# Performance work log

Measured on AMD Instinct MI355X. Metric: run time of the kernel, lower is better.

## Reference

```python
import jax, jax.numpy as jnp
import numpy as np

# param tuples: (vdecay, vth, grad_win(=threshold_adaptation), grad_amp, rate_scale)
HID = (0.5, 0.3, 0.3, 1.0, 1.0)
OUT = (0.5, 0.3, 0.3, 1.0, 1.0)

B, I, H, O, T = 128, 1024, 4096, 512, 100


def setup_inputs() -> dict:
    key = jax.random.key(0)
    k1, k2, k3 = jax.random.split(key, 3)
    return {
        "spike_data": jax.random.uniform(k1, (B, I, T), dtype=jnp.float32),
        "hid_spike0": jnp.zeros((B, H), jnp.float32),
        "hid_volt0": jnp.zeros((B, H), jnp.float32),
        "out_spike0": jnp.zeros((B, O), jnp.float32),
        "out_volt0": jnp.zeros((B, O), jnp.float32),
        "w_hid": jax.random.normal(k2, (H, I), dtype=jnp.float32) * 0.02,
        "w_out": jax.random.normal(k3, (O, H), dtype=jnp.float32) * 0.02,
        "batch_size": B,
        "spike_ts": T,
    }


def _spike(volt, p):
    vdecay, vth, grad_win, grad_amp, rate_scale = p
    scaled = rate_scale * volt
    dyn_vth = vth * jnp.tanh(grad_win * jnp.max(scaled))
    return (scaled > dyn_vth).astype(volt.dtype)


def reference(spike_data, hid_spike0, hid_volt0, out_spike0, out_volt0,
              w_hid, w_out, batch_size, spike_ts):
    x = jnp.transpose(spike_data.reshape(batch_size, I, spike_ts), (2, 0, 1))  # [T,B,I]

    def step(carry, xt):
        hs, hv, osp, ov = carry
        hv_new = hv * HID[0] * (1.0 - hs) + xt @ w_hid.T          # [B,H]
        hs_new = _spike(hv_new, HID)
        ov_new = ov * OUT[0] * (1.0 - osp) + hs_new @ w_out.T     # [B,O]
        os_new = _spike(ov_new, OUT)
        return (hs_new, hv_new, os_new, ov_new), os_new

    _, outs = jax.lax.scan(step, (hid_spike0, hid_volt0, out_spike0, out_volt0), x)
    return jnp.sum(outs, axis=0)  # [B,O]
```

## Files before the change

### kernel.cpp

```cpp
#include <hip/hip_runtime.h>
#include <math.h>
#include <stdint.h>

#define T_STEPS 100
#define B_DIM 128
#define I_DIM 1024
#define H_DIM 4096
#define O_DIM 512
#define T_CHUNK 20
#define HS_RING 21
#define HS_SLOT ((size_t)8*128*512)
#define OV_LAG 21
#define RING_S 40
#define TAIL_START 80
#define LEADER 255

typedef _Float16 f16x8 __attribute__((ext_vector_type(8)));
typedef _Float16 f16x4 __attribute__((ext_vector_type(4)));
typedef float    f32x4 __attribute__((ext_vector_type(4)));

#define AS1 __attribute__((address_space(1)))
#define AS3 __attribute__((address_space(3)))

#define ALOAD(p)    __hip_atomic_load((p), __ATOMIC_RELAXED, __HIP_MEMORY_SCOPE_AGENT)
#define ASTORE(p,v) __hip_atomic_store((p), (v), __ATOMIC_RELAXED, __HIP_MEMORY_SCOPE_AGENT)

__device__ __forceinline__ void gload_lds16(const _Float16* g, _Float16* l){
  __builtin_amdgcn_global_load_lds(
      (const AS1 unsigned*)(uintptr_t)g,
      (AS3 unsigned*)(unsigned)(uintptr_t)l, 16, 0, 0);
}

__device__ __forceinline__ unsigned fmap(float f){
  unsigned u = __float_as_uint(f);
  return (u & 0x80000000u) ? ~u : (u | 0x80000000u);
}
__device__ __forceinline__ float funmap(unsigned m){
  unsigned u = (m & 0x80000000u) ? (m & 0x7FFFFFFFu) : ~m;
  return __uint_as_float(u);
}
__device__ __forceinline__ float vth_of(unsigned m){
  return 0.3f * tanhf(0.3f * funmap(m));
}

__device__ __forceinline__ unsigned poll2max(const unsigned* base, int idx){
  const unsigned long long* p = (const unsigned long long*)base + idx;
  unsigned long long v = ALOAD(p);
  while (((unsigned)v) == 0u || ((unsigned)(v >> 32)) == 0u){
    __builtin_amdgcn_s_sleep(1);
    v = ALOAD(p);
  }
  unsigned lo = (unsigned)v, hi = (unsigned)(v >> 32);
  return lo > hi ? lo : hi;
}
__device__ __forceinline__ unsigned wred_umax(unsigned v){
  #pragma unroll
  for (int o = 32; o > 0; o >>= 1){
    unsigned t = (unsigned)__shfl_down((int)v, o);
    if (t > v) v = t;
  }
  return v;
}

__global__ __launch_bounds__(256) void init_kernel(float* hv, float* ovs,
                                                   uint32_t* cnt32,
                                                   unsigned* hmaxA, unsigned* omaxA,
                                                   unsigned* hflag, unsigned* oflag,
                                                   unsigned* otflag)
{
  int i = blockIdx.x * 256 + threadIdx.x;
  if (i < B_DIM*H_DIM) hv[i] = 0.f;
  if (i < B_DIM*O_DIM) ovs[i] = 0.f;
  if (i < B_DIM*O_DIM/4) cnt32[i] = 0u;
  if (i < 100*256) hflag[i] = 0u;
  if (i < 101*32)  oflag[i] = 0u;
  if (i < 20*128)  otflag[i] = 0u;
  if (i < 128){
    unsigned v = (i==0) ? 0x80000000u : 0u;
    hmaxA[i] = v; omaxA[i] = v;
  }
}

__global__ __launch_bounds__(256) void prep_x(const float* __restrict__ sp,
                                              _Float16* __restrict__ Ahi,
                                              _Float16* __restrict__ Alo, int t0)
{
  __shared__ float tile[32][16][10];
  const int b16 = blockIdx.x, kc = blockIdx.y, tz = blockIdx.z;
  for (int e = threadIdx.x; e < 5120; e += 256){
    int tt = e % 10, row = e / 10;
    int bb = row >> 5, ii = row & 31;
    tile[ii][bb][tt] =
      sp[((size_t)(b16*16+bb)*I_DIM + kc*32 + ii)*T_STEPS + t0 + tz*10 + tt];
  }
  __syncthreads();
  for (int u = threadIdx.x; u < 640; u += 256){
    int tl = u >> 6, l = u & 63, kg = l >> 4, r = l & 15;
    f16x8 hi, lo;
    #pragma unroll
    for (int e=0;e<8;e++){
      float x = tile[kg*8+e][r][tl] * 2048.f;
      _Float16 h = (_Float16)x;
      hi[e] = h;
      lo[e] = (_Float16)(x - (float)h);
    }
    int t_local = tz*10 + tl;
    size_t off = ((size_t)(t_local*8 + b16)*32 + kc)*512 + kg*128 + r*8;
    *(f16x8*)(Ahi + off) = hi;
    *(f16x8*)(Alo + off) = lo;
  }
}

__global__ __launch_bounds__(256) void prep_weights(
    const float* __restrict__ Wh, const float* __restrict__ Wo,
    _Float16* __restrict__ WHhi, _Float16* __restrict__ WHlo,
    _Float16* __restrict__ WOhi, _Float16* __restrict__ WOlo)
{
  const int blk = blockIdx.x;
  if (blk < 256){
    const int n16 = blk;
    for (int u = threadIdx.x; u < 2048; u += 256){
      int kc = u >> 6, l = u & 63, kg = l >> 4, r = l & 15;
      const float* src = Wh + (size_t)(n16*16 + r)*I_DIM + kc*32 + kg*8;
      f16x8 hi, lo;
      #pragma unroll
      for (int e=0;e<8;e++){
        float x = src[e] * 256.f;
        _Float16 h = (_Float16)x;
        hi[e] = h; lo[e] = (_Float16)(x - (float)h);
      }
      size_t off = ((size_t)n16*32 + kc)*512 + kg*128 + r*8;
      *(f16x8*)(WHhi + off) = hi;
      *(f16x8*)(WHlo + off) = lo;
    }
  } else {
    const int n16 = blk - 256;
    for (int u = threadIdx.x; u < 8192; u += 256){
      int kc = u >> 6, l = u & 63, kg = l >> 4, r = l & 15;
      const float* src = Wo + (size_t)(n16*16 + r)*H_DIM + kc*32 + kg*8;
      f16x8 hi, lo;
      #pragma unroll
      for (int e=0;e<8;e++){
        float x = src[e] * 256.f;
        _Float16 h = (_Float16)x;
        hi[e] = h; lo[e] = (_Float16)(x - (float)h);
      }
      size_t off = ((size_t)(n16*128 + kc))*512 + kg*128 + r*8;
      *(f16x8*)(WOhi + off) = hi;
      *(f16x8*)(WOlo + off) = lo;
    }
  }
}

__global__ __launch_bounds__(256, 2) void gemm1_mfma(
    const _Float16* __restrict__ Ahi, const _Float16* __restrict__ Alo,
    const _Float16* __restrict__ Bhi, const _Float16* __restrict__ Blo,
    float* __restrict__ G)
{
  __shared__ __align__(16) _Float16 lds[2][4][8][512];
  const int tid = threadIdx.x, wave = tid>>6, lane = tid&63;
  const int bn = blockIdx.x, bm = blockIdx.y;
  const int wm = wave>>1, wn = wave&1;

  const _Float16* srcbase = (wave==0)?Ahi:(wave==1)?Alo:(wave==2)?Bhi:Blo;
  const int r16b = ((wave<2) ? bm : bn)*8;
  const _Float16* gsrc = srcbase + (size_t)r16b*32*512 + lane*8;

  f32x4 acc[16];
  #pragma unroll
  for (int i=0;i<16;i++) acc[i] = (f32x4){0.f,0.f,0.f,0.f};

  #pragma unroll
  for (int q=0;q<8;q++)
    gload_lds16(gsrc + (size_t)q*32*512, &lds[0][wave][q][0]);

  for (int kc=0;kc<32;kc++){
    __syncthreads();
    if (kc < 31){
      #pragma unroll
      for (int q=0;q<8;q++)
        gload_lds16(gsrc + ((size_t)q*32 + kc+1)*512, &lds[(kc+1)&1][wave][q][0]);
    }
    const int cb = kc&1;
    f16x8 fAh[4], fAl[4], fBh[4], fBl[4];
    #pragma unroll
    for (int i=0;i<4;i++){
      fAh[i] = *(const f16x8*)&lds[cb][0][wm*4+i][lane*8];
      fAl[i] = *(const f16x8*)&lds[cb][1][wm*4+i][lane*8];
      fBh[i] = *(const f16x8*)&lds[cb][2][wn*4+i][lane*8];
      fBl[i] = *(const f16x8*)&lds[cb][3][wn*4+i][lane*8];
    }
    #pragma unroll
    for (int i=0;i<4;i++)
      #pragma unroll
      for (int j=0;j<4;j++)
        acc[i*4+j] = __builtin_amdgcn_mfma_f32_16x16x32_f16(fAh[i], fBh[j], acc[i*4+j], 0,0,0);
    #pragma unroll
    for (int i=0;i<4;i++)
      #pragma unroll
      for (int j=0;j<4;j++)
        acc[i*4+j] = __builtin_amdgcn_mfma_f32_16x16x32_f16(fAh[i], fBl[j], acc[i*4+j], 0,0,0);
    #pragma unroll
    for (int i=0;i<4;i++)
      #pragma unroll
      for (int j=0;j<4;j++)
        acc[i*4+j] = __builtin_amdgcn_mfma_f32_16x16x32_f16(fAl[i], fBh[j], acc[i*4+j], 0,0,0);
  }
  const int colw = lane&15, quad = lane>>4;
  const float sc = 1.f/(2048.f*256.f);
  float* eds = (float*)lds + wave*2048;
  __syncthreads();
  #pragma unroll
  for (int ih=0; ih<2; ih++){
    #pragma unroll
    for (int il=0; il<2; il++){
      int i = ih*2+il;
      #pragma unroll
      for (int j=0;j<4;j++)
        #pragma unroll
        for (int r=0;r<4;r++)
          eds[(il*16 + quad*4 + r)*64 + j*16 + colw] = acc[i*4+j][r]*sc;
    }
    #pragma unroll
    for (int rr8=0; rr8<8; rr8++){
      int row = rr8*4 + quad;
      float4 v = *(float4*)&eds[row*64 + colw*4];
      int m = bm*128 + wm*64 + ih*32 + row;
      int n = bn*128 + wn*64 + colw*4;
      *(float4*)&G[(size_t)m*H_DIM + n] = v;
    }
  }
}

__global__ __launch_bounds__(256) void hv_step(
    const float* __restrict__ Gs, float* __restrict__ hv,
    _Float16* __restrict__ hs_slot,
    const unsigned* __restrict__ hmax_t, unsigned* __restrict__ hmax_n, int t,
    const float* __restrict__ OGp, float* __restrict__ ovs,
    uchar4* __restrict__ cnt8, unsigned* __restrict__ omaxA, int ovt)
{
  __shared__ float red[4];
  const int tid = threadIdx.x, lane = tid&63, wv = tid>>6;

  if (blockIdx.x < 512){
    if (t > T_STEPS) return;
    const int gid = blockIdx.x*256 + tid;
    const int b = gid >> 10, h0 = (gid & 1023) << 2;
    const float vth = vth_of(*hmax_t);
    float4 h = *(const float4*)(hv + (size_t)gid*4);

    if (t > 0){
      const int kc = h0>>5, kg=(h0>>3)&3, e=h0&7, r=b&15, m16l=b>>4;
      f16x4 s;
      s[0]=(h.x>vth)?(_Float16)1:(_Float16)0; s[1]=(h.y>vth)?(_Float16)1:(_Float16)0;
      s[2]=(h.z>vth)?(_Float16)1:(_Float16)0; s[3]=(h.w>vth)?(_Float16)1:(_Float16)0;
      *(f16x4*)(hs_slot + ((size_t)m16l*128 + kc)*512 + kg*128 + r*8 + e) = s;
    }
    if (t < T_STEPS){
      float4 g = *(const float4*)(Gs + (size_t)gid*4);
      float4 o;
      o.x = (h.x>vth ? 0.f : 0.5f*h.x) + g.x;
      o.y = (h.y>vth ? 0.f : 0.5f*h.y) + g.y;
      o.z = (h.z>vth ? 0.f : 0.5f*h.z) + g.z;
      o.w = (h.w>vth ? 0.f : 0.5f*h.w) + g.w;
      *(float4*)(hv + (size_t)gid*4) = o;
      float lmax = fmaxf(fmaxf(o.x,o.y),fmaxf(o.z,o.w));
      #pragma unroll
      for (int off=32; off>0; off>>=1) lmax = fmaxf(lmax, __shfl_down(lmax, off));
      if (lane==0) red[wv] = lmax;
      __syncthreads();
      if (tid==0){
        float m = fmaxf(fmaxf(red[0],red[1]),fmaxf(red[2],red[3]));
        atomicMax(hmax_n, fmap(m));
      }
    }
  } else {
    if (ovt < 0 || ovt >= TAIL_START) return;
    const int f = (int)(blockIdx.x - 512)*256 + tid;
    const float vthp = vth_of(omaxA[ovt]);
    const int slot = ovt % RING_S;
    float lmax = -3.0e38f;
    #pragma unroll
    for (int q=0;q<4;q++){
      int o4 = f + q*4096;
      float4 v = *(const float4*)(ovs + (size_t)o4*4);
      uchar4 c = cnt8[o4];
      bool s0 = v.x > vthp, s1 = v.y > vthp, s2 = v.z > vthp, s3 = v.w > vthp;
      c.x += s0; c.y += s1; c.z += s2; c.w += s3;
      v.x = s0 ? 0.f : 0.5f*v.x;
      v.y = s1 ? 0.f : 0.5f*v.y;
      v.z = s2 ? 0.f : 0.5f*v.z;
      v.w = s3 ? 0.f : 0.5f*v.w;
      float4 g0 = *(const float4*)(OGp + ((size_t)slot*4+0)*(B_DIM*O_DIM) + (size_t)o4*4);
      float4 g1 = *(const float4*)(OGp + ((size_t)slot*4+1)*(B_DIM*O_DIM) + (size_t)o4*4);
      float4 g2 = *(const float4*)(OGp + ((size_t)slot*4+2)*(B_DIM*O_DIM) + (size_t)o4*4);
      float4 g3 = *(const float4*)(OGp + ((size_t)slot*4+3)*(B_DIM*O_DIM) + (size_t)o4*4);
      v.x += (g0.x+g1.x)+(g2.x+g3.x);
      v.y += (g0.y+g1.y)+(g2.y+g3.y);
      v.z += (g0.z+g1.z)+(g2.z+g3.z);
      v.w += (g0.w+g1.w)+(g2.w+g3.w);
      lmax = fmaxf(lmax, fmaxf(fmaxf(v.x,v.y),fmaxf(v.z,v.w)));
      *(float4*)(ovs + (size_t)o4*4) = v;
      cnt8[o4] = c;
    }
    #pragma unroll
    for (int off=32; off>0; off>>=1) lmax = fmaxf(lmax, __shfl_down(lmax, off));
    if (lane==0) red[wv] = lmax;
    __syncthreads();
    if (tid==0){
      float m = fmaxf(fmaxf(red[0],red[1]),fmaxf(red[2],red[3]));
      atomicMax(&omaxA[ovt+1], fmap(m));
    }
  }
}

__global__ __launch_bounds__(512) void hv_chunk(
    const float* __restrict__ Gs,
    float* __restrict__ hv,
    _Float16* __restrict__ HS,
    unsigned* __restrict__ hmaxA,
    const float* __restrict__ OGp, float* __restrict__ ovs,
    uchar4* __restrict__ cnt8, unsigned* __restrict__ omaxA,
    unsigned* __restrict__ hflag, unsigned* __restrict__ oflag,
    int t0, int nsteps)
{
  __shared__ float red[8], redo[8];
  __shared__ unsigned sredH[2];
  __shared__ unsigned sredO;
  const int tid = threadIdx.x, lane = tid&63, wv = tid>>6;
  const int blk = blockIdx.x;
  const int gid = blk*512 + tid;
  const int b = gid >> 10, h0 = (gid & 1023) << 2;
  const int kc = h0>>5, kg=(h0>>3)&3, e=h0&7, r=b&15, m16l=b>>4;
  const bool ovblk = blk < 32;
  const int ovt0 = t0 - OV_LAG;
  const bool rid = ovblk && (ovt0 >= 0);

  float4 h = *(const float4*)(hv + (size_t)gid*4);
  float4 vo = make_float4(0.f,0.f,0.f,0.f);
  unsigned cw = 0;
  if (ovblk){
    vo = *(const float4*)(ovs + (size_t)gid*4);
    uchar4 c0 = cnt8[gid];
    cw = (unsigned)c0.x | ((unsigned)c0.y<<8) | ((unsigned)c0.z<<16) | ((unsigned)c0.w<<24);
  }
  float4 g = *(const float4*)(Gs + (size_t)gid*4);
  unsigned hm_cur = hmaxA[t0];
  unsigned om_cur = rid ? omaxA[ovt0] : 0;

  float4 og0,og1,og2,og3;
  og0=og1=og2=og3=make_float4(0.f,0.f,0.f,0.f);
  if (rid){
    const int sl = ovt0 % RING_S;
    const float* base = OGp + (size_t)gid*4;
    og0 = *(const float4*)(base + (size_t)(sl*4+0)*(B_DIM*O_DIM));
    og1 = *(const float4*)(base + (size_t)(sl*4+1)*(B_DIM*O_DIM));
    og2 = *(const float4*)(base + (size_t)(sl*4+2)*(B_DIM*O_DIM));
    og3 = *(const float4*)(base + (size_t)(sl*4+3)*(B_DIM*O_DIM));
  }

  for (int j = 0; j < nsteps; j++){
    const int t = t0 + j;
    const int ovt = t - OV_LAG;
    const bool last = (j == nsteps-1);

    float4 gn = make_float4(0.f,0.f,0.f,0.f);
    if (!last && (t+1) < T_STEPS)
      gn = *(const float4*)(Gs + (size_t)(j+1)*(B_DIM*H_DIM) + (size_t)gid*4);
    float4 on0,on1,on2,on3;
    on0=on1=on2=on3=make_float4(0.f,0.f,0.f,0.f);
    if (rid && !last){
      const int sln = (ovt+1) % RING_S;
      const float* base = OGp + (size_t)gid*4;
      on0 = *(const float4*)(base + (size_t)(sln*4+0)*(B_DIM*O_DIM));
      on1 = *(const float4*)(base + (size_t)(sln*4+1)*(B_DIM*O_DIM));
      on2 = *(const float4*)(base + (size_t)(sln*4+2)*(B_DIM*O_DIM));
      on3 = *(const float4*)(base + (size_t)(sln*4+3)*(B_DIM*O_DIM));
    }

    const float vth = vth_of(hm_cur);
    {
      f16x4 s;
      s[0]=(h.x>vth)?(_Float16)1:(_Float16)0; s[1]=(h.y>vth)?(_Float16)1:(_Float16)0;
      s[2]=(h.z>vth)?(_Float16)1:(_Float16)0; s[3]=(h.w>vth)?(_Float16)1:(_Float16)0;
      _Float16* slotp = HS + (size_t)((t-1)%HS_RING)*HS_SLOT;
      *(f16x4*)(slotp + ((size_t)m16l*128 + kc)*512 + kg*128 + r*8 + e) = s;
    }
    float lmax = -3.0e38f;
    if (t < T_STEPS){
      h.x = (h.x>vth ? 0.f : 0.5f*h.x) + g.x;
      h.y = (h.y>vth ? 0.f : 0.5f*h.y) + g.y;
      h.z = (h.z>vth ? 0.f : 0.5f*h.z) + g.z;
      h.w = (h.w>vth ? 0.f : 0.5f*h.w) + g.w;
      lmax = fmaxf(fmaxf(h.x,h.y),fmaxf(h.z,h.w));
    }

    float omax_l = -3.0e38f;
    if (rid){
      const float vthp = vth_of(om_cur);
      bool s0 = vo.x > vthp, s1 = vo.y > vthp, s2 = vo.z > vthp, s3 = vo.w > vthp;
      cw += (s0?1u:0u) | (s1?(1u<<8):0u) | (s2?(1u<<16):0u) | (s3?(1u<<24):0u);
      vo.x = s0 ? 0.f : 0.5f*vo.x;
      vo.y = s1 ? 0.f : 0.5f*vo.y;
      vo.z = s2 ? 0.f : 0.5f*vo.z;
      vo.w = s3 ? 0.f : 0.5f*vo.w;
      vo.x += (og0.x+og1.x)+(og2.x+og3.x);
      vo.y += (og0.y+og1.y)+(og2.y+og3.y);
      vo.z += (og0.z+og1.z)+(og2.z+og3.z);
      vo.w += (og0.w+og1.w)+(og2.w+og3.w);
      omax_l = fmaxf(fmaxf(vo.x,vo.y),fmaxf(vo.z,vo.w));
    }

    #pragma unroll
    for (int off2=32; off2>0; off2>>=1) lmax = fmaxf(lmax, __shfl_down(lmax, off2));
    if (lane==0) red[wv] = lmax;
    if (rid){
      #pragma unroll
      for (int off2=32; off2>0; off2>>=1) omax_l = fmaxf(omax_l, __shfl_down(omax_l, off2));
      if (lane==0) redo[wv] = omax_l;
    }
    __syncthreads();

    if (tid == 0 && t < T_STEPS){
      float m = red[0];
      #pragma unroll
      for (int w2=1; w2<8; w2++) m = fmaxf(m, red[w2]);
      ASTORE(&hflag[(size_t)t*256 + blk], fmap(m));
    }
    if (tid == 0 && rid){
      float mo = redo[0];
      #pragma unroll
      for (int w2=1; w2<8; w2++) mo = fmaxf(mo, redo[w2]);
      ASTORE(&oflag[(size_t)ovt*32 + blk], fmap(mo));
    }

    if (!last){
      if (tid < 128){
        unsigned mx = poll2max(hflag + (size_t)t*256, tid);
        mx = wred_umax(mx);
        if (lane == 0) sredH[wv] = mx;
      }
      if (rid && tid >= 128 && tid < 192){
        unsigned mx = 0;
        if (tid < 144) mx = poll2max(oflag + (size_t)ovt*32, tid - 128);
        mx = wred_umax(mx);
        if (lane == 0) sredO = mx;
      }
      __syncthreads();
      { unsigned m0 = sredH[0], m1 = sredH[1];
        hm_cur = m0 > m1 ? m0 : m1; }
      if (rid) om_cur = sredO;
      if (blk == LEADER && tid == 0) ASTORE(&hmaxA[t+1], hm_cur);
      if (blk == 0 && rid && tid == 0) ASTORE(&omaxA[ovt+1], om_cur);
      g = gn;
      og0=on0; og1=on1; og2=on2; og3=on3;
    } else {
      if (blk == LEADER && t < T_STEPS){
        if (tid < 128){
          unsigned mx = poll2max(hflag + (size_t)t*256, tid);
          mx = wred_umax(mx);
          if (lane == 0) sredH[wv] = mx;
        }
        __syncthreads();
        if (tid == 0){
          unsigned m0 = sredH[0], m1 = sredH[1];
          ASTORE(&hmaxA[t+1], m0 > m1 ? m0 : m1);
        }
      }
      if (blk == 0 && rid){
        if (tid < 64){
          unsigned mx = 0;
          if (tid < 16) mx = poll2max(oflag + (size_t)ovt*32, tid);
          mx = wred_umax(mx);
          if (tid == 0) ASTORE(&omaxA[ovt+1], mx);
        }
      }
    }
  }

  *(float4*)(hv + (size_t)gid*4) = h;
  if (ovblk){
    *(float4*)(ovs + (size_t)gid*4) = vo;
    cnt8[gid] = make_uchar4((unsigned char)(cw & 0xffu),
                            (unsigned char)((cw>>8) & 0xffu),
                            (unsigned char)((cw>>16) & 0xffu),
                            (unsigned char)((cw>>24) & 0xffu));
  }
}

__global__ __launch_bounds__(256, 2) void gemm2_mfma(
    const _Float16* __restrict__ HS,
    const _Float16* __restrict__ WoHi, const _Float16* __restrict__ WoLo,
    float* __restrict__ OGp, int c)
{
  __shared__ __align__(16) _Float16 lds2[2][24][512];
  const int tid = threadIdx.x, wave = tid>>6, lane = tid&63;
  const int bn = blockIdx.x, bm = blockIdx.y, kh = blockIdx.z;
  const int s = c*T_CHUNK + bm, ring = s % HS_RING;
  const int wm = wave>>1, wn = wave&1;
  const int kc0 = kh*32;

  const _Float16* baseA = HS   + (size_t)ring*8*128*512 + lane*8;
  const _Float16* baseH = WoHi + (size_t)bn*8*128*512 + lane*8;
  const _Float16* baseL = WoLo + (size_t)bn*8*128*512 + lane*8;

  f32x4 acc[16];
  #pragma unroll
  for (int i=0;i<16;i++) acc[i] = (f32x4){0.f,0.f,0.f,0.f};

  #pragma unroll
  for (int i=0;i<6;i++){
    int f = wave*6 + i;
    const _Float16* g = (f<8)  ? baseA + ((size_t)f*128      + kc0)*512
                     : (f<16) ? baseH + ((size_t)(f-8)*128  + kc0)*512
                              : baseL + ((size_t)(f-16)*128 + kc0)*512;
    gload_lds16(g, &lds2[0][f][0]);
  }

  for (int k=0;k<32;k++){
    __syncthreads();
    if (k < 31){
      #pragma unroll
      for (int i=0;i<6;i++){
        int f = wave*6 + i;
        const _Float16* g = (f<8)  ? baseA + ((size_t)f*128      + kc0+k+1)*512
                         : (f<16) ? baseH + ((size_t)(f-8)*128  + kc0+k+1)*512
                                  : baseL + ((size_t)(f-16)*128 + kc0+k+1)*512;
        gload_lds16(g, &lds2[(k+1)&1][f][0]);
      }
    }
    const int cb = k&1;
    f16x8 fA[4], fH[4], fL[4];
    #pragma unroll
    for (int i=0;i<4;i++){
      fA[i] = *(const f16x8*)&lds2[cb][wm*4+i][lane*8];
      fH[i] = *(const f16x8*)&lds2[cb][8+wn*4+i][lane*8];
      fL[i] = *(const f16x8*)&lds2[cb][16+wn*4+i][lane*8];
    }
    #pragma unroll
    for (int i=0;i<4;i++)
      #pragma unroll
      for (int j=0;j<4;j++)
        acc[i*4+j] = __builtin_amdgcn_mfma_f32_16x16x32_f16(fA[i], fH[j], acc[i*4+j], 0,0,0);
    #pragma unroll
    for (int i=0;i<4;i++)
      #pragma unroll
      for (int j=0;j<4;j++)
        acc[i*4+j] = __builtin_amdgcn_mfma_f32_16x16x32_f16(fA[i], fL[j], acc[i*4+j], 0,0,0);
  }
  const int colw = lane&15, quad = lane>>4;
  const float sc = 1.f/256.f;
  float* eds = (float*)lds2 + wave*2048;
  __syncthreads();
  float* OGd = OGp + ((size_t)(s % RING_S)*4 + kh)*(B_DIM*O_DIM);
  #pragma unroll
  for (int ih=0; ih<2; ih++){
    #pragma unroll
    for (int il=0; il<2; il++){
      int i = ih*2+il;
      #pragma unroll
      for (int j=0;j<4;j++)
        #pragma unroll
        for (int r=0;r<4;r++)
          eds[(il*16 + quad*4 + r)*64 + j*16 + colw] = acc[i*4+j][r]*sc;
    }
    #pragma unroll
    for (int rr8=0; rr8<8; rr8++){
      int row = rr8*4 + quad;
      float4 v = *(float4*)&eds[row*64 + colw*4];
      int m = wm*64 + ih*32 + row;
      int n = bn*128 + wn*64 + colw*4;
      *(float4*)&OGd[(size_t)m*O_DIM + n] = v;
    }
  }
}

__global__ __launch_bounds__(128) void ov_tail(
    const float* __restrict__ OGp, const float* __restrict__ ovs,
    const uchar4* __restrict__ cnt8, const unsigned* __restrict__ omaxA,
    unsigned* __restrict__ otflag, float* __restrict__ out)
{
  __shared__ float red[2];
  __shared__ unsigned shm;
  const int tid = threadIdx.x, lane = tid&63, wv = tid>>6;
  const int f = blockIdx.x*128 + tid;
  float4 ov = *(const float4*)(ovs + (size_t)f*4);
  uchar4 c0 = cnt8[f];
  unsigned cw = (unsigned)c0.x | ((unsigned)c0.y<<8) | ((unsigned)c0.z<<16) | ((unsigned)c0.w<<24);
  unsigned om_cur = omaxA[TAIL_START];

  float4 og0,og1,og2,og3;
  {
    const int sl = TAIL_START % RING_S;
    const float* base = OGp + (size_t)f*4;
    og0 = *(const float4*)(base + (size_t)(sl*4+0)*(B_DIM*O_DIM));
    og1 = *(const float4*)(base + (size_t)(sl*4+1)*(B_DIM*O_DIM));
    og2 = *(const float4*)(base + (size_t)(sl*4+2)*(B_DIM*O_DIM));
    og3 = *(const float4*)(base + (size_t)(sl*4+3)*(B_DIM*O_DIM));
  }

  for (int ovt = TAIL_START; ovt <= T_STEPS; ovt++){
    float4 n0,n1,n2,n3;
    n0=n1=n2=n3=make_float4(0.f,0.f,0.f,0.f);
    if ((ovt+1) < T_STEPS){
      const int sl = (ovt+1) % RING_S;
      const float* base = OGp + (size_t)f*4;
      n0 = *(const float4*)(base + (size_t)(sl*4+0)*(B_DIM*O_DIM));
      n1 = *(const float4*)(base + (size_t)(sl*4+1)*(B_DIM*O_DIM));
      n2 = *(const float4*)(base + (size_t)(sl*4+2)*(B_DIM*O_DIM));
      n3 = *(const float4*)(base + (size_t)(sl*4+3)*(B_DIM*O_DIM));
    }
    const float vth = vth_of(om_cur);
    bool s0 = ov.x > vth, s1 = ov.y > vth, s2 = ov.z > vth, s3 = ov.w > vth;
    cw += (s0?1u:0u) | (s1?(1u<<8):0u) | (s2?(1u<<16):0u) | (s3?(1u<<24):0u);
    ov.x = s0 ? 0.f : 0.5f*ov.x;
    ov.y = s1 ? 0.f : 0.5f*ov.y;
    ov.z = s2 ? 0.f : 0.5f*ov.z;
    ov.w = s3 ? 0.f : 0.5f*ov.w;
    if (ovt == T_STEPS) break;
    ov.x += (og0.x+og1.x)+(og2.x+og3.x);
    ov.y += (og0.y+og1.y)+(og2.y+og3.y);
    ov.z += (og0.z+og1.z)+(og2.z+og3.z);
    ov.w += (og0.w+og1.w)+(og2.w+og3.w);
    float lmax = fmaxf(fmaxf(ov.x,ov.y),fmaxf(ov.z,ov.w));
    #pragma unroll
    for (int off=32; off>0; off>>=1) lmax = fmaxf(lmax, __shfl_down(lmax, off));
    if (lane==0) red[wv] = lmax;
    __syncthreads();
    if (tid==0)
      ASTORE(&otflag[(size_t)(ovt-TAIL_START)*128 + blockIdx.x],
             fmap(fmaxf(red[0], red[1])));
    if (tid < 64){
      unsigned mx = poll2max(otflag + (size_t)(ovt-TAIL_START)*128, tid);
      mx = wred_umax(mx);
      if (tid == 0) shm = mx;
    }
    __syncthreads();
    om_cur = shm;
    og0=n0; og1=n1; og2=n2; og3=n3;
  }
  *(float4*)(out + (size_t)f*4) = make_float4(
      (float)( cw        & 0xffu),
      (float)((cw >> 8)  & 0xffu),
      (float)((cw >> 16) & 0xffu),
      (float)((cw >> 24) & 0xffu));
}

extern "C" void kernel_launch(void* const* d_in, const int* in_sizes, int n_in,
                              void* d_out, int out_size, void* d_ws, size_t ws_size,
                              hipStream_t stream) {
  const float* spike = (const float*)d_in[0];
  const float* Wh    = (const float*)d_in[5];
  const float* Wo    = (const float*)d_in[6];
  float* out = (float*)d_out;

  char* ws = (char*)d_ws;
  size_t off = 0;
  _Float16* XAhi = (_Float16*)(ws+off); off += (size_t)T_CHUNK*B_DIM*I_DIM*2;
  _Float16* XAlo = (_Float16*)(ws+off); off += (size_t)T_CHUNK*B_DIM*I_DIM*2;
  _Float16* WHhi = (_Float16*)(ws+off); off += (size_t)H_DIM*I_DIM*2;
  _Float16* WHlo = (_Float16*)(ws+off); off += (size_t)H_DIM*I_DIM*2;
  _Float16* WOhi = (_Float16*)(ws+off); off += (size_t)O_DIM*H_DIM*2;
  _Float16* WOlo = (_Float16*)(ws+off); off += (size_t)O_DIM*H_DIM*2;
  float* G  = (float*)(ws+off);         off += (size_t)T_CHUNK*B_DIM*H_DIM*4;
  float* hv = (float*)(ws+off);         off += (size_t)B_DIM*H_DIM*4;
  _Float16* HS = (_Float16*)(ws+off);   off += (size_t)HS_RING*HS_SLOT*2;
  float* OGp = (float*)(ws+off);        off += (size_t)RING_S*4*B_DIM*O_DIM*4;
  float* ovs = (float*)(ws+off);        off += (size_t)B_DIM*O_DIM*4;
  uchar4* cnt8 = (uchar4*)(ws+off);     off += (size_t)B_DIM*O_DIM;
  unsigned* hmaxA = (unsigned*)(ws+off); off += 128*4;
  unsigned* omaxA = (unsigned*)(ws+off); off += 128*4;
  unsigned* hflag = (unsigned*)(ws+off); off += (size_t)100*256*4;
  unsigned* oflag = (unsigned*)(ws+off); off += (size_t)101*32*4;
  unsigned* otflag = (unsigned*)(ws+off); off += (size_t)20*128*4;
  (void)ws_size; (void)in_sizes; (void)n_in; (void)out_size;

  init_kernel<<<(B_DIM*H_DIM+255)/256, 256, 0, stream>>>(
      hv, ovs, (uint32_t*)cnt8, hmaxA, omaxA, hflag, oflag, otflag);
  prep_weights<<<288, 256, 0, stream>>>(Wh, Wo, WHhi, WHlo, WOhi, WOlo);

  for (int c = 0; c < T_STEPS/T_CHUNK; c++){
    prep_x<<<dim3(8,32,2), 256, 0, stream>>>(spike, XAhi, XAlo, c*T_CHUNK);
    gemm1_mfma<<<dim3(32, T_CHUNK), 256, 0, stream>>>(XAhi, XAlo, WHhi, WHlo, G);
    {
      int t = c*T_CHUNK;
      int ring = (t == 0) ? (HS_RING-1) : ((t-1) % HS_RING);
      hv_step<<<528, 256, 0, stream>>>(
          G, hv, HS + (size_t)ring*HS_SLOT,
          hmaxA + t, hmaxA + t + 1, t,
          OGp, ovs, cnt8, omaxA, t - OV_LAG);
    }
    if (c > 0)
      gemm2_mfma<<<dim3(4, T_CHUNK, 4), 256, 0, stream>>>(HS, WOhi, WOlo, OGp, c-1);
    {
      int nsteps = (c == T_STEPS/T_CHUNK - 1) ? T_CHUNK : (T_CHUNK - 1);
      hv_chunk<<<256, 512, 0, stream>>>(
          G + (size_t)B_DIM*H_DIM, hv, HS, hmaxA,
          OGp, ovs, cnt8, omaxA, hflag, oflag,
          c*T_CHUNK + 1, nsteps);
    }
  }
  gemm2_mfma<<<dim3(4, T_CHUNK, 4), 256, 0, stream>>>(HS, WOhi, WOlo, OGp, T_STEPS/T_CHUNK - 1);
  ov_tail<<<128, 128, 0, stream>>>(OGp, ovs, cnt8, omaxA, otflag, out);
}
```

Before: 1.236 ms.

## Pack hidden and output max flags into one 64-bit word, halve hv_chunk grid

The persistent hv_chunk kernel now runs 128 blocks of 1024 threads instead of 256 blocks of 512. Each block covers a 16-batch by 256-hidden tile, and the output-voltage work is spread across all blocks rather than the first 32. The per-step hidden max and output max flags are combined into one 64-bit word per block, so each step needs a single grid-wide poll over 128 flags instead of two separate polls. This is meant to cut cross-block barrier latency in the recurrent loop. The cost is larger blocks, which may hurt occupancy and latency hiding, and a remapped HS store layout.

```diff
diff --git a/kernel.cpp b/kernel.cpp
--- a/kernel.cpp
+++ b/kernel.cpp
@@ -13,7 +13,7 @@
 #define OV_LAG 21
 #define RING_S 40
 #define TAIL_START 80
-#define LEADER 255
+#define LEADER 127
 
 typedef _Float16 f16x8 __attribute__((ext_vector_type(8)));
 typedef _Float16 f16x4 __attribute__((ext_vector_type(4)));
@@ -65,15 +65,13 @@
 __global__ __launch_bounds__(256) void init_kernel(float* hv, float* ovs,
                                                    uint32_t* cnt32,
                                                    unsigned* hmaxA, unsigned* omaxA,
-                                                   unsigned* hflag, unsigned* oflag,
-                                                   unsigned* otflag)
+                                                   unsigned* hflag32, unsigned* otflag)
 {
   int i = blockIdx.x * 256 + threadIdx.x;
   if (i < B_DIM*H_DIM) hv[i] = 0.f;
   if (i < B_DIM*O_DIM) ovs[i] = 0.f;
   if (i < B_DIM*O_DIM/4) cnt32[i] = 0u;
-  if (i < 100*256) hflag[i] = 0u;
-  if (i < 101*32)  oflag[i] = 0u;
+  if (i < 101*256) hflag32[i] = 0u;
   if (i < 20*128)  otflag[i] = 0u;
   if (i < 128){
     unsigned v = (i==0) ? 0x80000000u : 0u;
@@ -314,45 +312,47 @@
   }
 }
 
-__global__ __launch_bounds__(512) void hv_chunk(
+__global__ __launch_bounds__(1024) void hv_chunk(
     const float* __restrict__ Gs,
     float* __restrict__ hv,
     _Float16* __restrict__ HS,
     unsigned* __restrict__ hmaxA,
     const float* __restrict__ OGp, float* __restrict__ ovs,
     uchar4* __restrict__ cnt8, unsigned* __restrict__ omaxA,
-    unsigned* __restrict__ hflag, unsigned* __restrict__ oflag,
+    unsigned long long* __restrict__ hflag,
     int t0, int nsteps)
 {
-  __shared__ float red[8], redo[8];
-  __shared__ unsigned sredH[2];
-  __shared__ unsigned sredO;
+  __shared__ float red[16], redo[2];
+  __shared__ unsigned sredL[2], sredH2[2];
   const int tid = threadIdx.x, lane = tid&63, wv = tid>>6;
   const int blk = blockIdx.x;
-  const int gid = blk*512 + tid;
-  const int b = gid >> 10, h0 = (gid & 1023) << 2;
-  const int kc = h0>>5, kg=(h0>>3)&3, e=h0&7, r=b&15, m16l=b>>4;
-  const bool ovblk = blk < 32;
+  const int B0 = blk >> 4, H0 = blk & 15;
+  const int b_off = tid >> 6, f4off = tid & 63;
+  const int f4idx = (B0*16 + b_off)*1024 + H0*64 + f4off;
+  const size_t hs_off = ((size_t)(B0*128 + H0*8 + (f4off>>3)))*512
+                      + (size_t)(((f4off>>1)&3)*128 + b_off*8 + (f4off&1)*4);
+  const bool ovth = tid < 128;
+  const int of4 = blk*128 + tid;
   const int ovt0 = t0 - OV_LAG;
-  const bool rid = ovblk && (ovt0 >= 0);
-
-  float4 h = *(const float4*)(hv + (size_t)gid*4);
+  const bool rid = (ovt0 >= 0);
+
+  float4 h = *(const float4*)(hv + (size_t)f4idx*4);
   float4 vo = make_float4(0.f,0.f,0.f,0.f);
   unsigned cw = 0;
-  if (ovblk){
-    vo = *(const float4*)(ovs + (size_t)gid*4);
-    uchar4 c0 = cnt8[gid];
+  if (rid && ovth){
+    vo = *(const float4*)(ovs + (size_t)of4*4);
+    uchar4 c0 = cnt8[of4];
     cw = (unsigned)c0.x | ((unsigned)c0.y<<8) | ((unsigned)c0.z<<16) | ((unsigned)c0.w<<24);
   }
-  float4 g = *(const float4*)(Gs + (size_t)gid*4);
+  float4 g = *(const float4*)(Gs + (size_t)f4idx*4);
   unsigned hm_cur = hmaxA[t0];
   unsigned om_cur = rid ? omaxA[ovt0] : 0;
 
   float4 og0,og1,og2,og3;
   og0=og1=og2=og3=make_float4(0.f,0.f,0.f,0.f);
-  if (rid){
+  if (rid && ovth){
     const int sl = ovt0 % RING_S;
-    const float* base = OGp + (size_t)gid*4;
+    const float* base = OGp + (size_t)of4*4;
     og0 = *(const float4*)(base + (size_t)(sl*4+0)*(B_DIM*O_DIM));
     og1 = *(const float4*)(base + (size_t)(sl*4+1)*(B_DIM*O_DIM));
     og2 = *(const float4*)(base + (size_t)(sl*4+2)*(B_DIM*O_DIM));
@@ -366,12 +366,12 @@
 
     float4 gn = make_float4(0.f,0.f,0.f,0.f);
     if (!last && (t+1) < T_STEPS)
-      gn = *(const float4*)(Gs + (size_t)(j+1)*(B_DIM*H_DIM) + (size_t)gid*4);
+      gn = *(const float4*)(Gs + (size_t)(j+1)*(B_DIM*H_DIM) + (size_t)f4idx*4);
     float4 on0,on1,on2,on3;
     on0=on1=on2=on3=make_float4(0.f,0.f,0.f,0.f);
-    if (rid && !last){
+    if (rid && ovth && !last){
       const int sln = (ovt+1) % RING_S;
-      const float* base = OGp + (size_t)gid*4;
+      const float* base = OGp + (size_t)of4*4;
       on0 = *(const float4*)(base + (size_t)(sln*4+0)*(B_DIM*O_DIM));
       on1 = *(const float4*)(base + (size_t)(sln*4+1)*(B_DIM*O_DIM));
       on2 = *(const float4*)(base + (size_t)(sln*4+2)*(B_DIM*O_DIM));
@@ -384,7 +384,7 @@
       s[0]=(h.x>vth)?(_Float16)1:(_Float16)0; s[1]=(h.y>vth)?(_Float16)1:(_Float16)0;
       s[2]=(h.z>vth)?(_Float16)1:(_Float16)0; s[3]=(h.w>vth)?(_Float16)1:(_Float16)0;
       _Float16* slotp = HS + (size_t)((t-1)%HS_RING)*HS_SLOT;
-      *(f16x4*)(slotp + ((size_t)m16l*128 + kc)*512 + kg*128 + r*8 + e) = s;
+      *(f16x4*)(slotp + hs_off) = s;
     }
     float lmax = -3.0e38f;
     if (t < T_STEPS){
@@ -396,7 +396,7 @@
     }
 
     float omax_l = -3.0e38f;
-    if (rid){
+    if (rid && ovth){
       const float vthp = vth_of(om_cur);
       bool s0 = vo.x > vthp, s1 = vo.y > vthp, s2 = vo.z > vthp, s3 = vo.w > vthp;
       cw += (s0?1u:0u) | (s1?(1u<<8):0u) | (s2?(1u<<16):0u) | (s3?(1u<<24):0u);
@@ -414,74 +414,59 @@
     #pragma unroll
     for (int off2=32; off2>0; off2>>=1) lmax = fmaxf(lmax, __shfl_down(lmax, off2));
     if (lane==0) red[wv] = lmax;
-    if (rid){
+    if (rid && wv < 2){
       #pragma unroll
       for (int off2=32; off2>0; off2>>=1) omax_l = fmaxf(omax_l, __shfl_down(omax_l, off2));
       if (lane==0) redo[wv] = omax_l;
     }
     __syncthreads();
 
-    if (tid == 0 && t < T_STEPS){
-      float m = red[0];
-      #pragma unroll
-      for (int w2=1; w2<8; w2++) m = fmaxf(m, red[w2]);
-      ASTORE(&hflag[(size_t)t*256 + blk], fmap(m));
-    }
-    if (tid == 0 && rid){
-      float mo = redo[0];
-      #pragma unroll
-      for (int w2=1; w2<8; w2++) mo = fmaxf(mo, redo[w2]);
-      ASTORE(&oflag[(size_t)ovt*32 + blk], fmap(mo));
-    }
-
-    if (!last){
+    if (tid == 0){
+      unsigned hp = 1u, op = 1u;
+      if (t < T_STEPS){
+        float m = red[0];
+        #pragma unroll
+        for (int w2=1; w2<16; w2++) m = fmaxf(m, red[w2]);
+        hp = fmap(m);
+      }
+      if (rid) op = fmap(fmaxf(redo[0], redo[1]));
+      ASTORE(&hflag[(size_t)t*128 + blk],
+             (unsigned long long)hp | ((unsigned long long)op << 32));
+    }
+
+    const bool doPoll = !last || (blk == LEADER && t < T_STEPS) || (blk == 0 && rid);
+    if (doPoll){
+      unsigned plo = 0, phi = 0;
       if (tid < 128){
-        unsigned mx = poll2max(hflag + (size_t)t*256, tid);
-        mx = wred_umax(mx);
-        if (lane == 0) sredH[wv] = mx;
+        const unsigned long long* fp = hflag + (size_t)t*128 + tid;
+        unsigned long long v = ALOAD(fp);
+        while (((unsigned)v) == 0u){
+          __builtin_amdgcn_s_sleep(1);
+          v = ALOAD(fp);
+        }
+        plo = (unsigned)v; phi = (unsigned)(v >> 32);
       }
-      if (rid && tid >= 128 && tid < 192){
-        unsigned mx = 0;
-        if (tid < 144) mx = poll2max(oflag + (size_t)ovt*32, tid - 128);
-        mx = wred_umax(mx);
-        if (lane == 0) sredO = mx;
+      plo = wred_umax(plo);
+      phi = wred_umax(phi);
+      if (lane == 0 && wv < 2){ sredL[wv] = plo; sredH2[wv] = phi; }
+      __syncthreads();
+      unsigned hm2 = sredL[0] > sredL[1] ? sredL[0] : sredL[1];
+      unsigned om2 = sredH2[0] > sredH2[1] ? sredH2[0] : sredH2[1];
+      if (!last){
+        hm_cur = hm2;
+        if (rid) om_cur = om2;
       }
-      __syncthreads();
-      { unsigned m0 = sredH[0], m1 = sredH[1];
-        hm_cur = m0 > m1 ? m0 : m1; }
-      if (rid) om_cur = sredO;
-      if (blk == LEADER && tid == 0) ASTORE(&hmaxA[t+1], hm_cur);
-      if (blk == 0 && rid && tid == 0) ASTORE(&omaxA[ovt+1], om_cur);
-      g = gn;
-      og0=on0; og1=on1; og2=on2; og3=on3;
-    } else {
-      if (blk == LEADER && t < T_STEPS){
-        if (tid < 128){
-          unsigned mx = poll2max(hflag + (size_t)t*256, tid);
-          mx = wred_umax(mx);
-          if (lane == 0) sredH[wv] = mx;
-        }
-        __syncthreads();
-        if (tid == 0){
-          unsigned m0 = sredH[0], m1 = sredH[1];
-          ASTORE(&hmaxA[t+1], m0 > m1 ? m0 : m1);
-        }
-      }
-      if (blk == 0 && rid){
-        if (tid < 64){
-          unsigned mx = 0;
-          if (tid < 16) mx = poll2max(oflag + (size_t)ovt*32, tid);
-          mx = wred_umax(mx);
-          if (tid == 0) ASTORE(&omaxA[ovt+1], mx);
-        }
-      }
-    }
-  }
-
-  *(float4*)(hv + (size_t)gid*4) = h;
-  if (ovblk){
-    *(float4*)(ovs + (size_t)gid*4) = vo;
-    cnt8[gid] = make_uchar4((unsigned char)(cw & 0xffu),
+      if (blk == LEADER && tid == 0 && t < T_STEPS) ASTORE(&hmaxA[t+1], hm2);
+      if (blk == 0 && rid && tid == 0 && ovt >= 0) ASTORE(&omaxA[ovt+1], om2);
+    }
+    g = gn;
+    og0=on0; og1=on1; og2=on2; og3=on3;
+  }
+
+  *(float4*)(hv + (size_t)f4idx*4) = h;
+  if (rid && ovth){
+    *(float4*)(ovs + (size_t)of4*4) = vo;
+    cnt8[of4] = make_uchar4((unsigned char)(cw & 0xffu),
                             (unsigned char)((cw>>8) & 0xffu),
                             (unsigned char)((cw>>16) & 0xffu),
                             (unsigned char)((cw>>24) & 0xffu));
@@ -670,13 +655,12 @@
   uchar4* cnt8 = (uchar4*)(ws+off);     off += (size_t)B_DIM*O_DIM;
   unsigned* hmaxA = (unsigned*)(ws+off); off += 128*4;
   unsigned* omaxA = (unsigned*)(ws+off); off += 128*4;
-  unsigned* hflag = (unsigned*)(ws+off); off += (size_t)100*256*4;
-  unsigned* oflag = (unsigned*)(ws+off); off += (size_t)101*32*4;
+  unsigned long long* hflag = (unsigned long long*)(ws+off); off += (size_t)101*128*8;
   unsigned* otflag = (unsigned*)(ws+off); off += (size_t)20*128*4;
   (void)ws_size; (void)in_sizes; (void)n_in; (void)out_size;
 
   init_kernel<<<(B_DIM*H_DIM+255)/256, 256, 0, stream>>>(
-      hv, ovs, (uint32_t*)cnt8, hmaxA, omaxA, hflag, oflag, otflag);
+      hv, ovs, (uint32_t*)cnt8, hmaxA, omaxA, (unsigned*)hflag, otflag);
   prep_weights<<<288, 256, 0, stream>>>(Wh, Wo, WHhi, WHlo, WOhi, WOlo);
 
   for (int c = 0; c < T_STEPS/T_CHUNK; c++){
@@ -694,9 +678,9 @@
       gemm2_mfma<<<dim3(4, T_CHUNK, 4), 256, 0, stream>>>(HS, WOhi, WOlo, OGp, c-1);
     {
       int nsteps = (c == T_STEPS/T_CHUNK - 1) ? T_CHUNK : (T_CHUNK - 1);
-      hv_chunk<<<256, 512, 0, stream>>>(
+      hv_chunk<<<128, 1024, 0, stream>>>(
           G + (size_t)B_DIM*H_DIM, hv, HS, hmaxA,
-          OGp, ovs, cnt8, omaxA, hflag, oflag,
+          OGp, ovs, cnt8, omaxA, hflag,
           c*T_CHUNK + 1, nsteps);
     }
   }
```

After: 1.142 ms. 7.6% less time.
